# Kernel tuning notes

Hardware: AMD Instinct MI355X
Metric: run time of the kernel (lower is better)

The kernel has to match this reference:

```python
import jax, jax.numpy as jnp
import numpy as np

I = 4  # input size
H = 4  # hidden size


def setup_inputs() -> dict:
    key = jax.random.key(0)
    ks = jax.random.split(key, 7)
    T, B = 2048, 8192
    s = 1.0 / np.sqrt(H)  # torch LSTM/Linear init scale
    x = jax.random.normal(ks[0], (T, B, I), dtype=jnp.float32)
    w_ih = jax.random.uniform(ks[1], (4 * H, I), minval=-s, maxval=s, dtype=jnp.float32)
    w_hh = jax.random.uniform(ks[2], (4 * H, H), minval=-s, maxval=s, dtype=jnp.float32)
    b_ih = jax.random.uniform(ks[3], (4 * H,), minval=-s, maxval=s, dtype=jnp.float32)
    b_hh = jax.random.uniform(ks[4], (4 * H,), minval=-s, maxval=s, dtype=jnp.float32)
    w_lin = jax.random.uniform(ks[5], (1, H), minval=-0.5, maxval=0.5, dtype=jnp.float32)
    b_lin = jax.random.uniform(ks[6], (1,), minval=-0.5, maxval=0.5, dtype=jnp.float32)
    return {"x": x, "w_ih": w_ih, "w_hh": w_hh, "b_ih": b_ih, "b_hh": b_hh,
            "w_lin": w_lin, "b_lin": b_lin}


def _lstm_scan(x, w_ih, w_hh, b_ih, b_hh):
    # x: (T, B, I). PyTorch gate order: i, f, g, o.
    T, B, _ = x.shape
    b = b_ih + b_hh  # (4H,)
    # Precompute input projections for all timesteps: (T, B, 4H)
    xg = jnp.einsum('tbi,gi->tbg', x, w_ih) + b

    def step(carry, xg_t):
        h, c = carry  # (B, H) each
        gates = xg_t + h @ w_hh.T  # (B, 4H)
        i, f, g, o = jnp.split(gates, 4, axis=-1)
        i = jax.nn.sigmoid(i)
        f = jax.nn.sigmoid(f)
        g = jnp.tanh(g)
        o = jax.nn.sigmoid(o)
        c = f * c + i * g
        h = o * jnp.tanh(c)
        return (h, c), h

    h0 = jnp.zeros((B, H), dtype=x.dtype)
    c0 = jnp.zeros((B, H), dtype=x.dtype)
    _, hs = jax.lax.scan(step, (h0, c0), xg)
    return hs  # (T, B, H)


def reference(x, w_ih, w_hh, b_ih, b_hh, w_lin, b_lin):
    hs = _lstm_scan(x, w_ih, w_hh, b_ih, b_hh)           # (T, B, H)
    out = jnp.einsum('tbh,oh->tbo', hs, w_lin) + b_lin   # (T, B, 1)
    return jax.nn.sigmoid(out)
```

## Files before the change

kernel.cpp:

```cpp
#include <hip/hip_runtime.h>

#define T_DIM 2048
#define B_DIM 8192

__device__ __forceinline__ float dpp_qxor1(float v) {
  int i = __float_as_int(v);
  return __int_as_float(__builtin_amdgcn_update_dpp(i, i, 0xB1, 0xF, 0xF, false));
}
__device__ __forceinline__ float dpp_qxor2(float v) {
  int i = __float_as_int(v);
  return __int_as_float(__builtin_amdgcn_update_dpp(i, i, 0x4E, 0xF, 0xF, false));
}
__device__ __forceinline__ float dpp_qxor3(float v) {
  int i = __float_as_int(v);
  return __int_as_float(__builtin_amdgcn_update_dpp(i, i, 0x1B, 0xF, 0xF, false));
}
__device__ __forceinline__ float dpp_hmirror(float v) {
  int i = __float_as_int(v);
  return __int_as_float(__builtin_amdgcn_update_dpp(i, i, 0x141, 0xF, 0xF, false));
}

__global__ __launch_bounds__(256) void lstm_scan_kernel(
    const float* __restrict__ x,
    const float* __restrict__ w_ih, const float* __restrict__ w_hh,
    const float* __restrict__ b_ih, const float* __restrict__ b_hh,
    const float* __restrict__ w_lin, const float* __restrict__ b_lin,
    float* __restrict__ out)
{
  const int tid = blockIdx.x * blockDim.x + threadIdx.x;
  const int l = tid & 7;
  const int b = tid >> 3;
  const int half1 = (l >> 2) & 1;
  const int e = (l & 3) ^ (half1 ? 3 : 0);

  const int rA = half1 * 4 + e;
  const int rB = 8 + half1 * 4 + e;

  const float L2E = 1.4426950408889634f;
  const float cm2 = -2.0f * L2E;
  const float sclA = -L2E;
  const float sclB = half1 ? -L2E : -2.0f * L2E;

  float wihA[4], whhA[4], wihB[4], whhB[4];
  #pragma unroll
  for (int k = 0; k < 4; ++k) {
    const int j = e ^ k;
    wihA[k] = sclA * w_ih[rA * 4 + j];
    whhA[k] = sclA * w_hh[rA * 4 + j];
    wihB[k] = sclB * w_ih[rB * 4 + j];
    whhB[k] = sclB * w_hh[rB * 4 + j];
  }
  const float biasA = sclA * (b_ih[rA] + b_hh[rA]);
  const float biasB = sclB * (b_ih[rB] + b_hh[rB]);
  const float sB = half1 ? 1.0f : 2.0f * cm2;
  const float oB = half1 ? 0.0f : -cm2;
  const float wlo  = -L2E * w_lin[e];
  const float blin = -L2E * b_lin[0];

  float ct = 0.0f;
  float h0 = 0.0f, h1 = 0.0f, h2 = 0.0f, h3 = 0.0f;
  float accK = 0.0f;

  const int XS = B_DIM * 4;
  const int xoff = b * 4 + e;
  const int ooff = b + l * B_DIM;

  float r0[8], r1[8];
  float xaA0[8], xaB0[8], xaA1[8], xaB1[8];

  auto load8 = [&](float (&dst)[8], int tt) {
    const int base = xoff + tt * XS;
    #pragma unroll
    for (int k = 0; k < 8; ++k) dst[k] = x[base + k * XS];
  };

  auto proj1 = [&](float xe, float& oA, float& oBv) {
    const float xv1 = dpp_qxor1(xe);
    const float xv2 = dpp_qxor2(xe);
    const float xv3 = dpp_qxor3(xe);
    float a = fmaf(wihA[0], xe, biasA);
    a = fmaf(wihA[1], xv1, a);
    a = fmaf(wihA[2], xv2, a);
    a = fmaf(wihA[3], xv3, a);
    oA = a;
    float bb = fmaf(wihB[0], xe, biasB);
    bb = fmaf(wihB[1], xv1, bb);
    bb = fmaf(wihB[2], xv2, bb);
    bb = fmaf(wihB[3], xv3, bb);
    oBv = bb;
  };

  auto step8 = [&](int t0, float (&xaA)[8], float (&xaB)[8],
                   float (&raw)[8], float (&xnA)[8], float (&xnB)[8]) {
    #pragma unroll
    for (int k = 0; k < 8; ++k) {
      float uA = fmaf(whhA[0], h0, xaA[k]);
      uA = fmaf(whhA[1], h1, uA);
      const float vA = fmaf(whhA[3], h3, whhA[2] * h2);
      const float accA = uA + vA;
      float uB = fmaf(whhB[0], h0, xaB[k]);
      uB = fmaf(whhB[1], h1, uB);
      const float vB = fmaf(whhB[3], h3, whhB[2] * h2);
      const float accB = uB + vB;

      const float aA = __builtin_amdgcn_rcpf(1.0f + __builtin_amdgcn_exp2f(accA));
      const float yB = __builtin_amdgcn_rcpf(1.0f + __builtin_amdgcn_exp2f(accB));
      const float aB = fmaf(sB, yB, oB);

      const float Z = half1 ? aA : aA * aB;
      const float W = dpp_hmirror(Z);
      const float F = half1 ? Z : W;
      const float P = half1 ? W : Z;
      ct = fmaf(F, ct, P);

      const float zc = __builtin_amdgcn_exp2f(ct);
      const float rc = __builtin_amdgcn_rcpf(1.0f + zc);
      const float Ox = dpp_hmirror(aB);
      const float ov = half1 ? aB : Ox;
      const float tc = fmaf(2.0f, rc, -1.0f);
      const float hn = ov * tc;

      h0 = hn;
      h1 = dpp_qxor1(hn);
      h2 = dpp_qxor2(hn);
      h3 = dpp_qxor3(hn);

      float m = wlo * hn;
      m += dpp_qxor1(m);
      m += dpp_qxor2(m);
      accK = (l == k) ? m : accK;

      proj1(raw[k], xnA[k], xnB[k]);
    }
    const float z = __builtin_amdgcn_exp2f(accK + blin);
    out[ooff + t0 * B_DIM] = __builtin_amdgcn_rcpf(1.0f + z);
  };

  load8(r0, 0);
  load8(r1, 8);
  #pragma unroll
  for (int k = 0; k < 8; ++k) proj1(r0[k], xaA0[k], xaB0[k]);

  for (int t0 = 0; t0 < T_DIM; t0 += 16) {
    load8(r0, (t0 + 16) & (T_DIM - 1));
    step8(t0,     xaA0, xaB0, r1, xaA1, xaB1);
    load8(r1, (t0 + 24) & (T_DIM - 1));
    step8(t0 + 8, xaA1, xaB1, r0, xaA0, xaB0);
  }
}

extern "C" void kernel_launch(void* const* d_in, const int* in_sizes, int n_in,
                              void* d_out, int out_size, void* d_ws, size_t ws_size,
                              hipStream_t stream) {
  const float* x     = (const float*)d_in[0];
  const float* w_ih  = (const float*)d_in[1];
  const float* w_hh  = (const float*)d_in[2];
  const float* b_ih  = (const float*)d_in[3];
  const float* b_hh  = (const float*)d_in[4];
  const float* w_lin = (const float*)d_in[5];
  const float* b_lin = (const float*)d_in[6];
  float* out = (float*)d_out;

  const int threads = B_DIM * 8;
  dim3 block(256);
  dim3 grid(threads / 256);
  hipLaunchKernelGGL(lstm_scan_kernel, grid, block, 0, stream,
                     x, w_ih, w_hh, b_ih, b_hh, w_lin, b_lin, out);
}
```

Baseline: 283.2 us.

## Split LSTM into producer/consumer warps with LDS double-buffered input projections

Each block now pairs four recurrence waves with four helper waves. The helpers load x, compute the input projections into a double-buffered LDS array, and also compute and store the output head from hidden states written back to LDS. Recurrence waves get raised priority and only run the serial gate chain, which moves global loads, projection FMAs and output stores off the critical path. In exchange it adds block-wide barriers every 8 timesteps, LDS traffic, and uses twice the threads per batch element.

```diff
diff --git a/kernel.cpp b/kernel.cpp
--- a/kernel.cpp
+++ b/kernel.cpp
@@ -2,6 +2,8 @@
 
 #define T_DIM 2048
 #define B_DIM 8192
+#define PH    256
+#define SPH   8
 
 __device__ __forceinline__ float dpp_qxor1(float v) {
   int i = __float_as_int(v);
@@ -20,132 +22,164 @@
   return __int_as_float(__builtin_amdgcn_update_dpp(i, i, 0x141, 0xF, 0xF, false));
 }
 
-__global__ __launch_bounds__(256) void lstm_scan_kernel(
+__global__ __launch_bounds__(512) void lstm_pc_kernel(
     const float* __restrict__ x,
     const float* __restrict__ w_ih, const float* __restrict__ w_hh,
     const float* __restrict__ b_ih, const float* __restrict__ b_hh,
     const float* __restrict__ w_lin, const float* __restrict__ b_lin,
     float* __restrict__ out)
 {
-  const int tid = blockIdx.x * blockDim.x + threadIdx.x;
-  const int l = tid & 7;
-  const int b = tid >> 3;
+  __shared__ float xaBuf[2][4][64][18];
+  __shared__ float hnBuf[2][4][64][9];
+
+  const int tid  = threadIdx.x;
+  const int wid  = tid >> 6;
+  const int lane = tid & 63;
+  const int pair = wid & 3;
+
+  const float L2E = 1.4426950408889634f;
+  const float cm2 = -2.0f * L2E;
+
+  const int l = lane & 7;
   const int half1 = (l >> 2) & 1;
   const int e = (l & 3) ^ (half1 ? 3 : 0);
-
+  const int grp = lane >> 3;
   const int rA = half1 * 4 + e;
   const int rB = 8 + half1 * 4 + e;
-
-  const float L2E = 1.4426950408889634f;
-  const float cm2 = -2.0f * L2E;
   const float sclA = -L2E;
   const float sclB = half1 ? -L2E : -2.0f * L2E;
 
-  float wihA[4], whhA[4], wihB[4], whhB[4];
-  #pragma unroll
-  for (int k = 0; k < 4; ++k) {
-    const int j = e ^ k;
-    wihA[k] = sclA * w_ih[rA * 4 + j];
-    whhA[k] = sclA * w_hh[rA * 4 + j];
-    wihB[k] = sclB * w_ih[rB * 4 + j];
-    whhB[k] = sclB * w_hh[rB * 4 + j];
-  }
-  const float biasA = sclA * (b_ih[rA] + b_hh[rA]);
-  const float biasB = sclB * (b_ih[rB] + b_hh[rB]);
-  const float sB = half1 ? 1.0f : 2.0f * cm2;
-  const float oB = half1 ? 0.0f : -cm2;
-  const float wlo  = -L2E * w_lin[e];
-  const float blin = -L2E * b_lin[0];
-
-  float ct = 0.0f;
-  float h0 = 0.0f, h1 = 0.0f, h2 = 0.0f, h3 = 0.0f;
-  float accK = 0.0f;
-
-  const int XS = B_DIM * 4;
-  const int xoff = b * 4 + e;
-  const int ooff = b + l * B_DIM;
-
-  float r0[8], r1[8];
-  float xaA0[8], xaB0[8], xaA1[8], xaB1[8];
-
-  auto load8 = [&](float (&dst)[8], int tt) {
-    const int base = xoff + tt * XS;
+  if (wid < 4) {
+    __builtin_amdgcn_s_setprio(1);
+    float whhA[4], whhB[4];
     #pragma unroll
-    for (int k = 0; k < 8; ++k) dst[k] = x[base + k * XS];
-  };
-
-  auto proj1 = [&](float xe, float& oA, float& oBv) {
-    const float xv1 = dpp_qxor1(xe);
-    const float xv2 = dpp_qxor2(xe);
-    const float xv3 = dpp_qxor3(xe);
-    float a = fmaf(wihA[0], xe, biasA);
-    a = fmaf(wihA[1], xv1, a);
-    a = fmaf(wihA[2], xv2, a);
-    a = fmaf(wihA[3], xv3, a);
-    oA = a;
-    float bb = fmaf(wihB[0], xe, biasB);
-    bb = fmaf(wihB[1], xv1, bb);
-    bb = fmaf(wihB[2], xv2, bb);
-    bb = fmaf(wihB[3], xv3, bb);
-    oBv = bb;
-  };
-
-  auto step8 = [&](int t0, float (&xaA)[8], float (&xaB)[8],
-                   float (&raw)[8], float (&xnA)[8], float (&xnB)[8]) {
+    for (int k = 0; k < 4; ++k) {
+      const int j = e ^ k;
+      whhA[k] = sclA * w_hh[rA * 4 + j];
+      whhB[k] = sclB * w_hh[rB * 4 + j];
+    }
+    const float sB = half1 ? 1.0f : 2.0f * cm2;
+    const float oB = half1 ? 0.0f : -cm2;
+    float ct = 0.0f, h0 = 0.0f, h1 = 0.0f, h2 = 0.0f, h3 = 0.0f;
+
+    __syncthreads();
+
+    for (int p = 0; p < PH; ++p) {
+      const int d = p & 1;
+      float xaA[SPH], xaB[SPH];
+      #pragma unroll
+      for (int k = 0; k < SPH; ++k) {
+        xaA[k] = xaBuf[d][pair][lane][2 * k];
+        xaB[k] = xaBuf[d][pair][lane][2 * k + 1];
+      }
+      #pragma unroll
+      for (int k = 0; k < SPH; ++k) {
+        float uA = fmaf(whhA[0], h0, xaA[k]);
+        uA = fmaf(whhA[1], h1, uA);
+        uA = fmaf(whhA[2], h2, uA);
+        uA = fmaf(whhA[3], h3, uA);
+        float uB = fmaf(whhB[0], h0, xaB[k]);
+        uB = fmaf(whhB[1], h1, uB);
+        uB = fmaf(whhB[2], h2, uB);
+        uB = fmaf(whhB[3], h3, uB);
+        const float aA = __builtin_amdgcn_rcpf(1.0f + __builtin_amdgcn_exp2f(uA));
+        const float yB = __builtin_amdgcn_rcpf(1.0f + __builtin_amdgcn_exp2f(uB));
+        const float aB = fmaf(sB, yB, oB);
+        const float Z = half1 ? aA : aA * aB;
+        const float W = dpp_hmirror(Z);
+        const float F = half1 ? Z : W;
+        const float P = half1 ? W : Z;
+        ct = fmaf(F, ct, P);
+        const float zc = __builtin_amdgcn_exp2f(ct);
+        const float rc = __builtin_amdgcn_rcpf(1.0f + zc);
+        const float Ox = dpp_hmirror(aB);
+        const float ov = half1 ? aB : Ox;
+        const float tc = fmaf(2.0f, rc, -1.0f);
+        const float hn = ov * tc;
+        h0 = hn;
+        h1 = dpp_qxor1(hn);
+        h2 = dpp_qxor2(hn);
+        h3 = dpp_qxor3(hn);
+        hnBuf[d][pair][lane][k] = hn;
+      }
+      __syncthreads();
+    }
+  } else {
+    const int b = blockIdx.x * 32 + pair * 8 + grp;
+    float wihA[4], wihB[4];
     #pragma unroll
-    for (int k = 0; k < 8; ++k) {
-      float uA = fmaf(whhA[0], h0, xaA[k]);
-      uA = fmaf(whhA[1], h1, uA);
-      const float vA = fmaf(whhA[3], h3, whhA[2] * h2);
-      const float accA = uA + vA;
-      float uB = fmaf(whhB[0], h0, xaB[k]);
-      uB = fmaf(whhB[1], h1, uB);
-      const float vB = fmaf(whhB[3], h3, whhB[2] * h2);
-      const float accB = uB + vB;
-
-      const float aA = __builtin_amdgcn_rcpf(1.0f + __builtin_amdgcn_exp2f(accA));
-      const float yB = __builtin_amdgcn_rcpf(1.0f + __builtin_amdgcn_exp2f(accB));
-      const float aB = fmaf(sB, yB, oB);
-
-      const float Z = half1 ? aA : aA * aB;
-      const float W = dpp_hmirror(Z);
-      const float F = half1 ? Z : W;
-      const float P = half1 ? W : Z;
-      ct = fmaf(F, ct, P);
-
-      const float zc = __builtin_amdgcn_exp2f(ct);
-      const float rc = __builtin_amdgcn_rcpf(1.0f + zc);
-      const float Ox = dpp_hmirror(aB);
-      const float ov = half1 ? aB : Ox;
-      const float tc = fmaf(2.0f, rc, -1.0f);
-      const float hn = ov * tc;
-
-      h0 = hn;
-      h1 = dpp_qxor1(hn);
-      h2 = dpp_qxor2(hn);
-      h3 = dpp_qxor3(hn);
-
-      float m = wlo * hn;
-      m += dpp_qxor1(m);
-      m += dpp_qxor2(m);
-      accK = (l == k) ? m : accK;
-
-      proj1(raw[k], xnA[k], xnB[k]);
-    }
-    const float z = __builtin_amdgcn_exp2f(accK + blin);
-    out[ooff + t0 * B_DIM] = __builtin_amdgcn_rcpf(1.0f + z);
-  };
-
-  load8(r0, 0);
-  load8(r1, 8);
-  #pragma unroll
-  for (int k = 0; k < 8; ++k) proj1(r0[k], xaA0[k], xaB0[k]);
-
-  for (int t0 = 0; t0 < T_DIM; t0 += 16) {
-    load8(r0, (t0 + 16) & (T_DIM - 1));
-    step8(t0,     xaA0, xaB0, r1, xaA1, xaB1);
-    load8(r1, (t0 + 24) & (T_DIM - 1));
-    step8(t0 + 8, xaA1, xaB1, r0, xaA0, xaB0);
+    for (int k = 0; k < 4; ++k) {
+      const int j = e ^ k;
+      wihA[k] = sclA * w_ih[rA * 4 + j];
+      wihB[k] = sclB * w_ih[rB * 4 + j];
+    }
+    const float biasA = sclA * (b_ih[rA] + b_hh[rA]);
+    const float biasB = sclB * (b_ih[rB] + b_hh[rB]);
+    const int og = lane & 7, oj = lane >> 3;
+    const int ob = blockIdx.x * 32 + pair * 8 + og;
+    float wl[4];
+    #pragma unroll
+    for (int j = 0; j < 4; ++j) wl[j] = -L2E * w_lin[j];
+    const float blin = -L2E * b_lin[0];
+
+    const int XS = B_DIM * 4;
+    const int xoff = b * 4 + e;
+
+    float xc[SPH], xn[SPH];
+
+    auto load8 = [&](float (&dst)[SPH], int ph) {
+      const int base = xoff + ((ph & (PH - 1)) * SPH) * XS;
+      #pragma unroll
+      for (int k = 0; k < SPH; ++k) dst[k] = x[base + k * XS];
+    };
+    auto projWrite = [&](const float (&xr)[SPH], int dd) {
+      #pragma unroll
+      for (int k = 0; k < SPH; ++k) {
+        const float xe = xr[k];
+        const float x1 = dpp_qxor1(xe);
+        const float x2 = dpp_qxor2(xe);
+        const float x3 = dpp_qxor3(xe);
+        float a = fmaf(wihA[0], xe, biasA);
+        a = fmaf(wihA[1], x1, a);
+        a = fmaf(wihA[2], x2, a);
+        a = fmaf(wihA[3], x3, a);
+        float bb = fmaf(wihB[0], xe, biasB);
+        bb = fmaf(wihB[1], x1, bb);
+        bb = fmaf(wihB[2], x2, bb);
+        bb = fmaf(wihB[3], x3, bb);
+        xaBuf[dd][pair][lane][2 * k]     = a;
+        xaBuf[dd][pair][lane][2 * k + 1] = bb;
+      }
+    };
+    auto headStore = [&](int p, int dh) {
+      const float v0 = hnBuf[dh][pair][og * 8 + 0][oj];
+      const float v1 = hnBuf[dh][pair][og * 8 + 1][oj];
+      const float v2 = hnBuf[dh][pair][og * 8 + 2][oj];
+      const float v3 = hnBuf[dh][pair][og * 8 + 3][oj];
+      float m = fmaf(wl[0], v0, blin);
+      m = fmaf(wl[1], v1, m);
+      m = fmaf(wl[2], v2, m);
+      m = fmaf(wl[3], v3, m);
+      const float o = __builtin_amdgcn_rcpf(1.0f + __builtin_amdgcn_exp2f(m));
+      out[(size_t)(p * SPH + oj) * B_DIM + ob] = o;
+    };
+
+    load8(xc, 0);
+    projWrite(xc, 0);
+    load8(xn, 1);
+    __syncthreads();
+
+    for (int pp = 0; pp < PH; pp += 2) {
+      projWrite(xn, 1);
+      load8(xc, pp + 2);
+      if (pp > 0) headStore(pp - 1, 1);
+      __syncthreads();
+      projWrite(xc, 0);
+      load8(xn, pp + 3);
+      headStore(pp, 0);
+      __syncthreads();
+    }
+    headStore(PH - 1, 1);
   }
 }
 
@@ -161,9 +195,8 @@
   const float* b_lin = (const float*)d_in[6];
   float* out = (float*)d_out;
 
-  const int threads = B_DIM * 8;
-  dim3 block(256);
-  dim3 grid(threads / 256);
-  hipLaunchKernelGGL(lstm_scan_kernel, grid, block, 0, stream,
+  dim3 block(512);
+  dim3 grid(B_DIM / 32);
+  hipLaunchKernelGGL(lstm_pc_kernel, grid, block, 0, stream,
                      x, w_ih, w_hh, b_ih, b_hh, w_lin, b_lin, out);
 }
```

Measured after the change: 248.9 us. 1.14x faster.
